# Performance work log

Measured on AMD Instinct MI355X. Metric: run time of the kernel, lower is better.

## Reference

```python
import jax, jax.numpy as jnp
import numpy as np


def setup_inputs() -> dict:
    key = jax.random.key(0)
    ks = jax.random.split(key, 7)
    b, t, c = 2, 2048, 1024
    s = 0.02  # keep pre-softmax logits in a sane range
    return {
        "query": jax.random.normal(ks[0], (b, t, c), jnp.float32),
        "key": jax.random.normal(ks[1], (b, t, c), jnp.float32),
        "value": jax.random.normal(ks[2], (b, t, c), jnp.float32),
        "in_proj_w": jax.random.normal(ks[3], (3 * c, c), jnp.float32) * s,
        "in_proj_b": jax.random.normal(ks[4], (3 * c,), jnp.float32) * s,
        "out_proj_w": jax.random.normal(ks[5], (c, c), jnp.float32) * s,
        "out_proj_b": jax.random.normal(ks[6], (c,), jnp.float32) * s,
        "window_size": 128,
    }


def reference(query, key, value, in_proj_w, in_proj_b, out_proj_w, out_proj_b, window_size):
    num_heads = 16
    b, t, c = query.shape
    hd = c // num_heads
    wq, wk, wv = in_proj_w[:c], in_proj_w[c:2 * c], in_proj_w[2 * c:]
    bq, bk, bv = in_proj_b[:c], in_proj_b[c:2 * c], in_proj_b[2 * c:]
    # project and split heads: [b, h, t, hd]
    q = (query @ wq.T + bq).reshape(b, t, num_heads, hd).transpose(0, 2, 1, 3)
    k = (key @ wk.T + bk).reshape(b, t, num_heads, hd).transpose(0, 2, 1, 3)
    v = (value @ wv.T + bv).reshape(b, t, num_heads, hd).transpose(0, 2, 1, 3)
    # NOTE: torch adds a *float* attn_mask to the logits. The original mask is
    # 1.0 inside the sliding window, 0.0 outside -- an additive +1 bias, NOT -inf.
    idx = jnp.arange(t)
    band = (jnp.abs(idx[:, None] - idx[None, :]) <= window_size).astype(q.dtype)  # [t, t]
    scale = 1.0 / jnp.sqrt(jnp.asarray(hd, q.dtype))
    logits = jnp.einsum("bhqd,bhkd->bhqk", q * scale, k) + band  # [b,h,t,t]
    attn = jax.nn.softmax(logits, axis=-1)
    out = jnp.einsum("bhqk,bhkd->bhqd", attn, v)  # [b,h,t,hd]
    out = out.transpose(0, 2, 1, 3).reshape(b, t, c)
    return out @ out_proj_w.T + out_proj_b
```

## Files before the change

### kernel.cpp

```cpp
#include <hip/hip_runtime.h>

typedef __attribute__((ext_vector_type(8)))  short short8;
typedef __attribute__((ext_vector_type(4)))  float f32x4;
typedef __attribute__((ext_vector_type(16))) float f32x16;

constexpr int B  = 2;
constexpr int T  = 2048;
constexpr int C  = 1024;
constexpr int H  = 16;
constexpr int HD = 64;

__device__ inline unsigned bf16rne(float a){
  unsigned u = __builtin_bit_cast(unsigned, a);
  u += 0x7fffu + ((u >> 16) & 1u);
  return u >> 16;
}
__device__ inline unsigned bf16pair(float a, float b){
  unsigned ua = __builtin_bit_cast(unsigned, a); ua += 0x7fffu + ((ua >> 16) & 1u);
  unsigned ub = __builtin_bit_cast(unsigned, b); ub += 0x7fffu + ((ub >> 16) & 1u);
  return (ua >> 16) | (ub & 0xffff0000u);
}
__device__ inline void gll16(const void* g, void* l){
  __builtin_amdgcn_global_load_lds(
      (const __attribute__((address_space(1))) unsigned*)g,
      (__attribute__((address_space(3))) unsigned*)l, 16, 0, 0);
}
__device__ inline float exp2f_(float x){
#if __has_builtin(__builtin_amdgcn_exp2f)
  return __builtin_amdgcn_exp2f(x);
#else
  return __builtin_exp2f(x);
#endif
}

__global__ void convert_k(const float* __restrict__ ipw, const float* __restrict__ opw,
                          const float* __restrict__ q, const float* __restrict__ k,
                          const float* __restrict__ v, unsigned* __restrict__ dst)
{
  const int i = blockIdx.x * 256 + threadIdx.x;
  const long e = (long)i * 4;
  const float* src; long off;
  if      (e <  3145728) { src = ipw; off = e; }
  else if (e <  4194304) { src = opw; off = e - 3145728; }
  else if (e <  8388608) { src = q;   off = e - 4194304; }
  else if (e < 12582912) { src = k;   off = e - 8388608; }
  else                   { src = v;   off = e - 12582912; }
  const float4 x = *(const float4*)(src + off);
  dst[i*2+0] = bf16pair(x.x, x.y);
  dst[i*2+1] = bf16pair(x.z, x.w);
}

template<int MODE>
__global__ __launch_bounds__(256, 2) void gemm_k(
    const unsigned short* __restrict__ A0, const unsigned short* __restrict__ A1,
    const unsigned short* __restrict__ A2,
    const unsigned short* __restrict__ Wb, const float* __restrict__ bias,
    unsigned short* __restrict__ Qb, unsigned short* __restrict__ Kf,
    unsigned short* __restrict__ Vf, float* __restrict__ outF)
{
  __shared__ __align__(16) char gsm[32768];
  unsigned short* As = (unsigned short*)gsm;
  unsigned short* Bs = (unsigned short*)(gsm + 16384);

  const int tid  = threadIdx.x, lane = tid & 63, wv = tid >> 6;
  const int wm   = wv & 1, wn = wv >> 1;
  const int bn   = blockIdx.x, bm = blockIdx.y;
  const int m16  = lane & 15, quad = lane >> 4;

  const int which = (MODE == 0) ? (bn >> 3) : 0;
  const unsigned short* A = (which == 0) ? A0 : (which == 1 ? A1 : A2);

  f32x4 acc[4][4];
#pragma unroll
  for (int i = 0; i < 4; i++)
#pragma unroll
    for (int j = 0; j < 4; j++) acc[i][j] = (f32x4){0.f, 0.f, 0.f, 0.f};

  const int srow = (lane >> 3);
  const int skp  = (lane & 7) * 8;

  for (int k0 = 0; k0 < 1024; k0 += 64) {
    __syncthreads();
#pragma unroll
    for (int p = 0; p < 4; p++) {
      const int row = wv*32 + p*8 + srow;
      gll16(A  + (size_t)(bm*128 + row)*1024 + k0 + skp, (char*)As + (wv*4+p)*1024);
      gll16(Wb + (size_t)(bn*128 + row)*1024 + k0 + skp, (char*)Bs + (wv*4+p)*1024);
    }
    __syncthreads();

    short8 af[2][4], bf2[2][4];
#pragma unroll
    for (int kh = 0; kh < 2; kh++) {
#pragma unroll
      for (int i = 0; i < 4; i++)
        af[kh][i] = *(const short8*)((const char*)As + (wm*64 + i*16 + m16)*128 + kh*64 + quad*16);
#pragma unroll
      for (int j = 0; j < 4; j++)
        bf2[kh][j] = *(const short8*)((const char*)Bs + (wn*64 + j*16 + m16)*128 + kh*64 + quad*16);
    }
#pragma unroll
    for (int kh = 0; kh < 2; kh++)
#pragma unroll
      for (int i = 0; i < 4; i++)
#pragma unroll
        for (int j = 0; j < 4; j++)
          acc[i][j] = __builtin_amdgcn_mfma_f32_16x16x32_bf16(af[kh][i], bf2[kh][j], acc[i][j], 0,0,0);
  }

  if constexpr (MODE == 1) {
#pragma unroll
    for (int j = 0; j < 4; j++) {
      const int n_e = bn*128 + wn*64 + j*16 + m16;
      const float bj = bias[n_e];
#pragma unroll
      for (int i = 0; i < 4; i++) {
        const int mbase = bm*128 + wm*64 + i*16 + quad*4;
#pragma unroll
        for (int r = 0; r < 4; r++)
          outF[(size_t)(mbase + r) * 1024 + n_e] = acc[i][j][r] + bj;
      }
    }
  } else {
    __syncthreads();
    float* Ls = (float*)gsm;
    const int hbase = (bn & 7) * 2;
    const int b = bm >> 4;
    const int tbase = (bm & 15) * 128;
    if (which < 2) {
#pragma unroll
      for (int j = 0; j < 4; ++j) {
        const float bj = bias[bn*128 + wn*64 + j*16 + m16];
#pragma unroll
        for (int i = 0; i < 4; ++i) {
          const int m0 = wm*64 + i*16 + quad*4;
#pragma unroll
          for (int r = 0; r < 4; ++r)
            Ls[(m0 + r)*36 + wn*16 + m16] = acc[i][j][r] + bj;
        }
        __syncthreads();
#pragma unroll
        for (int r2 = 0; r2 < 2; ++r2) {
          const int v = r2*256 + tid;
          const int m = v & 127, seg = v >> 7;
          const int wn2 = seg >> 1;
          const float* src = &Ls[m*36 + wn2*16 + (seg & 1)*8];
          const float4 f0 = *(const float4*)src;
          const float4 f1 = *(const float4*)(src + 4);
          uint4 st;
          st.x = bf16pair(f0.x, f0.y); st.y = bf16pair(f0.z, f0.w);
          st.z = bf16pair(f1.x, f1.y); st.w = bf16pair(f1.z, f1.w);
          const int bhh = b*16 + hbase + wn2;
          if (which == 0) {
            const int d0 = j*16 + (seg & 1)*8;
            *(uint4*)&Qb[((size_t)(bhh*2048) + tbase + m)*64 + d0] = st;
          } else {
            const int kt = (tbase + m) >> 6;
            const int wkk = (m >> 5) & 1, ln2 = m & 31;
            const int h2 = seg & 1;
            uint4* dp = (uint4*)Kf + ((size_t)(bhh*32 + kt)*8 + j*2 + wkk)*64 + h2*32 + ln2;
            *dp = st;
          }
        }
        __syncthreads();
      }
    } else {
#pragma unroll
      for (int j = 0; j < 4; ++j) {
        const float bj = bias[bn*128 + wn*64 + j*16 + m16];
        const int col = wn*16 + m16;
#pragma unroll
        for (int i = 0; i < 4; ++i) {
          f32x4 tv = acc[i][j];
          tv[0] += bj; tv[1] += bj; tv[2] += bj; tv[3] += bj;
          *(f32x4*)&Ls[col*132 + wm*64 + i*16 + quad*4] = tv;
        }
        __syncthreads();
#pragma unroll
        for (int r2 = 0; r2 < 2; ++r2) {
          const int v = r2*256 + tid;
          const int n = v >> 4, mseg = v & 15;
          const float* src = &Ls[n*132 + mseg*8];
          const float4 f0 = *(const float4*)src;
          const float4 f1 = *(const float4*)(src + 4);
          uint4 st;
          st.x = bf16pair(f0.x, f0.y); st.y = bf16pair(f0.z, f0.w);
          st.z = bf16pair(f1.x, f1.y); st.w = bf16pair(f1.z, f1.w);
          const int d = j*16 + (n & 15);
          const int bhh = b*16 + hbase + (n >> 4);
          const int t0 = tbase + mseg*8;
          const int kt = t0 >> 6, tc = (t0 & 63) >> 3;
          const int wkk = tc >> 2, cc = (tc >> 1) & 1, h2 = tc & 1;
          const int dt = d >> 5, ln2 = d & 31;
          uint4* dp = (uint4*)Vf + (size_t)(bhh*32 + kt)*512 + dt*256 + cc*128 + wkk*64 + h2*32 + ln2;
          *dp = st;
        }
        __syncthreads();
      }
    }
  }
}

__global__ __launch_bounds__(256, 2) void attn_k(
    const unsigned short* __restrict__ Qb, const unsigned short* __restrict__ Kf,
    const unsigned short* __restrict__ Vf, const int* __restrict__ wptr,
    unsigned short* __restrict__ ctx)
{
  __shared__ __align__(16) char smem[16896];
  float* Om   = (float*)smem;
  float* lbuf = (float*)(smem + 16384);

  const int tid = threadIdx.x, lane = tid & 63, wv = tid >> 6;
  const int wq = wv >> 1, wk = wv & 1;
  const int h = lane >> 5, ln = lane & 31;
  const bool hs = (h == 1);
  const int bh = blockIdx.x, qt = blockIdx.y;
  const int win = *wptr;
  const int q0 = qt * 64 + wq * 32;
  const size_t hb = (size_t)bh * T * HD;

  constexpr float LOG2E = 1.44269504f;
  constexpr float C1    = 0.125f * LOG2E;

  short8 qf[4];
#pragma unroll
  for (int s = 0; s < 4; s++)
    qf[s] = *(const short8*)(Qb + hb + (size_t)(q0 + ln)*64 + s*16 + h*8);

  short8 onesv;
#pragma unroll
  for (int jj = 0; jj < 8; jj++) onesv[jj] = (short)0x3F80;

  f32x16 O0, O1, Lacc, Zv;
#pragma unroll
  for (int r = 0; r < 16; r++) { O0[r] = 0.f; O1[r] = 0.f; Lacc[r] = 0.f; Zv[r] = 0.f; }
  const int tq = q0 + ln;

  const uint4* kbase = (const uint4*)Kf + (size_t)bh*32*512 + wk*64 + lane;
  const uint4* vbase = (const uint4*)Vf + (size_t)bh*32*512 + wk*64 + lane;

  uint4 kA[4], vA[4], kB[4], vB[4];
#pragma unroll
  for (int s = 0; s < 4; s++) kA[s] = kbase[s*128];
#pragma unroll
  for (int u = 0; u < 4; u++) vA[u] = vbase[(u >> 1)*256 + (u & 1)*128];

  auto body = [&](int kt, uint4 (&ka)[4], uint4 (&va)[4]) {
    f32x16 st;
#pragma unroll
    for (int s = 0; s < 4; s++) {
      const short8 kf2 = __builtin_bit_cast(short8, ka[s]);
      st = __builtin_amdgcn_mfma_f32_32x32x16_bf16(kf2, qf[s], (s == 0 ? Zv : st), 0, 0, 0);
    }

    const int kb = kt*64 + wk*32;
    int sep = 0;
    if (kb > q0 + 31) sep = kb - (q0 + 31);
    else if (q0 > kb + 31) sep = q0 - (kb + 31);
    const int d1 = kb + 31 - q0, d2 = q0 + 31 - kb;
    const int dmax = max(d1 < 0 ? -d1 : d1, d2 < 0 ? -d2 : d2);

    float pr[16];
    if (sep > win) {
#pragma unroll
      for (int r = 0; r < 16; r++) pr[r] = exp2f_(st[r] * C1);
    } else if (dmax <= win) {
#pragma unroll
      for (int r = 0; r < 16; r++) pr[r] = exp2f_(__builtin_fmaf(st[r], C1, LOG2E));
    } else {
      const int tkb = kb + 4*h;
#pragma unroll
      for (int r = 0; r < 16; r++) {
        const int tk = tkb + (r & 3) + 8*(r >> 2);
        int dd = tq - tk; dd = dd < 0 ? -dd : dd;
        pr[r] = exp2f_(__builtin_fmaf(st[r], C1, dd <= win ? LOG2E : 0.0f));
      }
    }

    unsigned pk[8];
#pragma unroll
    for (int g = 0; g < 8; g++)
      pk[g] = __builtin_amdgcn_perm(__builtin_bit_cast(unsigned, pr[2*g+1]),
                                    __builtin_bit_cast(unsigned, pr[2*g]),
                                    0x07060302u);

#pragma unroll
    for (int c = 0; c < 2; c++) {
      const unsigned sh0 = (unsigned)__shfl_xor((int)pk[4*c+0], 32, 64);
      const unsigned sh1 = (unsigned)__shfl_xor((int)pk[4*c+1], 32, 64);
      const unsigned sh2 = (unsigned)__shfl_xor((int)pk[4*c+2], 32, 64);
      const unsigned sh3 = (unsigned)__shfl_xor((int)pk[4*c+3], 32, 64);
      union { unsigned u[4]; short8 v; } P;
      P.u[0] = hs ? sh2 : pk[4*c+0];
      P.u[1] = hs ? sh3 : pk[4*c+1];
      P.u[2] = hs ? pk[4*c+2] : sh0;
      P.u[3] = hs ? pk[4*c+3] : sh1;
#pragma unroll
      for (int dt = 0; dt < 2; dt++) {
        const short8 vf2 = __builtin_bit_cast(short8, va[dt*2 + c]);
        if (dt == 0) O0 = __builtin_amdgcn_mfma_f32_32x32x16_bf16(P.v, vf2, O0, 0,0,0);
        else         O1 = __builtin_amdgcn_mfma_f32_32x32x16_bf16(P.v, vf2, O1, 0,0,0);
      }
      Lacc = __builtin_amdgcn_mfma_f32_32x32x16_bf16(P.v, onesv, Lacc, 0,0,0);
    }
  };

  for (int kt = 0; kt < 32; kt += 2) {
    {
      const size_t o = (size_t)(kt + 1) * 512;
#pragma unroll
      for (int s = 0; s < 4; s++) kB[s] = kbase[o + s*128];
#pragma unroll
      for (int u = 0; u < 4; u++) vB[u] = vbase[o + (u >> 1)*256 + (u & 1)*128];
    }
    body(kt, kA, vA);
    if (kt + 2 < 32) {
      const size_t o = (size_t)(kt + 2) * 512;
#pragma unroll
      for (int s = 0; s < 4; s++) kA[s] = kbase[o + s*128];
#pragma unroll
      for (int u = 0; u < 4; u++) vA[u] = vbase[o + (u >> 1)*256 + (u & 1)*128];
    }
    body(kt + 1, kB, vB);
  }

  __syncthreads();
  if (wk == 1) {
#pragma unroll
    for (int r = 0; r < 16; r++) {
      Om[wq*2048 + r*64 + lane]        = O0[r];
      Om[wq*2048 + (16 + r)*64 + lane] = O1[r];
    }
    if (ln == 0) {
#pragma unroll
      for (int r = 0; r < 16; r++)
        lbuf[wq*32 + (r & 3) + 8*(r >> 2) + 4*h] = Lacc[r];
    }
  }
  __syncthreads();
  if (wk == 0) {
    const int b = bh >> 4, hh = bh & 15;
#pragma unroll
    for (int r = 0; r < 16; r++) {
      const int qrow = (r & 3) + 8*(r >> 2) + 4*h;
      const float lt = Lacc[r] + lbuf[wq*32 + qrow];
      const float linv = 1.0f / lt;
      const int t = q0 + qrow;
      const float o0 = (O0[r] + Om[wq*2048 + r*64 + lane]) * linv;
      const float o1 = (O1[r] + Om[wq*2048 + (16 + r)*64 + lane]) * linv;
      unsigned short* cp = ctx + (size_t)(b*2048 + t)*1024 + hh*64;
      cp[ln]      = (unsigned short)bf16rne(o0);
      cp[32 + ln] = (unsigned short)bf16rne(o1);
    }
  }
}

extern "C" void kernel_launch(void* const* d_in, const int* in_sizes, int n_in,
                              void* d_out, int out_size, void* d_ws, size_t ws_size,
                              hipStream_t stream)
{
  const float* query = (const float*)d_in[0];
  const float* key   = (const float*)d_in[1];
  const float* value = (const float*)d_in[2];
  const float* ipw   = (const float*)d_in[3];
  const float* ipb   = (const float*)d_in[4];
  const float* opw   = (const float*)d_in[5];
  const float* opb   = (const float*)d_in[6];
  const int*   win   = (const int*)d_in[7];

  char* ws = (char*)d_ws;
  unsigned short* Winbf  = (unsigned short*)(ws);
  unsigned short* Woutbf = (unsigned short*)(ws + 6291456);
  unsigned short* Qin    = (unsigned short*)(ws + 8388608);
  unsigned short* Kin    = (unsigned short*)(ws + 16777216);
  unsigned short* Vin    = (unsigned short*)(ws + 25165824);
  unsigned short* Qb     = (unsigned short*)(ws + 33554432);
  unsigned short* Kf     = (unsigned short*)(ws + 41943040);
  unsigned short* Vf     = (unsigned short*)(ws + 50331648);
  unsigned short* ctx    = (unsigned short*)(ws + 58720256);

  convert_k<<<16384, 256, 0, stream>>>(ipw, opw, query, key, value, (unsigned*)ws);

  gemm_k<0><<<dim3(24, 32), 256, 0, stream>>>(
      Qin, Kin, Vin, Winbf, ipb, Qb, Kf, Vf, nullptr);

  attn_k<<<dim3(32, 32), 256, 0, stream>>>(Qb, Kf, Vf, win, ctx);

  gemm_k<1><<<dim3(8, 32), 256, 0, stream>>>(
      ctx, ctx, ctx, Woutbf, opb, nullptr, nullptr, nullptr, (float*)d_out);
}
```

Baseline: 229.8 us.

## Shrink GEMM k-tiles, split out-proj GEMM, fold softmax scale into K, raise occupancy

The QKV GEMM's K step drops from 64 to 32, which cuts LDS to about 19KB, and launch bounds rise to three blocks per CU. The output projection moves to its own kernel with 128x64 tiles, doubling the grid from 256 to 512 blocks so more CUs are busy. The softmax scale times log2e is folded into K and its bias at projection time, which removes a multiply per logit in attention. Attention drops the double-buffered K/V registers in favour of single buffers prefetched within each iteration, freeing registers for higher occupancy at the cost of less latency hiding.

```diff
diff --git a/kernel.cpp b/kernel.cpp
--- a/kernel.cpp
+++ b/kernel.cpp
@@ -50,24 +50,23 @@
   dst[i*2+1] = bf16pair(x.z, x.w);
 }
 
-template<int MODE>
-__global__ __launch_bounds__(256, 2) void gemm_k(
+__global__ __launch_bounds__(256, 3) void gemm_qkv(
     const unsigned short* __restrict__ A0, const unsigned short* __restrict__ A1,
     const unsigned short* __restrict__ A2,
     const unsigned short* __restrict__ Wb, const float* __restrict__ bias,
     unsigned short* __restrict__ Qb, unsigned short* __restrict__ Kf,
-    unsigned short* __restrict__ Vf, float* __restrict__ outF)
+    unsigned short* __restrict__ Vf)
 {
-  __shared__ __align__(16) char gsm[32768];
+  __shared__ __align__(16) char gsm[18944];
   unsigned short* As = (unsigned short*)gsm;
-  unsigned short* Bs = (unsigned short*)(gsm + 16384);
+  unsigned short* Bs = (unsigned short*)(gsm + 8192);
 
   const int tid  = threadIdx.x, lane = tid & 63, wv = tid >> 6;
   const int wm   = wv & 1, wn = wv >> 1;
   const int bn   = blockIdx.x, bm = blockIdx.y;
   const int m16  = lane & 15, quad = lane >> 4;
 
-  const int which = (MODE == 0) ? (bn >> 3) : 0;
+  const int which = bn >> 3;
   const unsigned short* A = (which == 0) ? A0 : (which == 1 ? A1 : A2);
 
   f32x4 acc[4][4];
@@ -76,132 +75,172 @@
 #pragma unroll
     for (int j = 0; j < 4; j++) acc[i][j] = (f32x4){0.f, 0.f, 0.f, 0.f};
 
-  const int srow = (lane >> 3);
-  const int skp  = (lane & 7) * 8;
-
-  for (int k0 = 0; k0 < 1024; k0 += 64) {
+  const int srow = wv * 32 + (lane >> 2);
+  const int skp  = (lane & 3) * 8;
+
+  for (int k0 = 0; k0 < 1024; k0 += 32) {
     __syncthreads();
 #pragma unroll
-    for (int p = 0; p < 4; p++) {
-      const int row = wv*32 + p*8 + srow;
-      gll16(A  + (size_t)(bm*128 + row)*1024 + k0 + skp, (char*)As + (wv*4+p)*1024);
-      gll16(Wb + (size_t)(bn*128 + row)*1024 + k0 + skp, (char*)Bs + (wv*4+p)*1024);
+    for (int p = 0; p < 2; p++) {
+      gll16(A  + (size_t)(bm*128 + srow + p*16)*1024 + k0 + skp, (char*)As + wv*2048 + p*1024);
+      gll16(Wb + (size_t)(bn*128 + srow + p*16)*1024 + k0 + skp, (char*)Bs + wv*2048 + p*1024);
     }
     __syncthreads();
 
-    short8 af[2][4], bf2[2][4];
-#pragma unroll
-    for (int kh = 0; kh < 2; kh++) {
-#pragma unroll
-      for (int i = 0; i < 4; i++)
-        af[kh][i] = *(const short8*)((const char*)As + (wm*64 + i*16 + m16)*128 + kh*64 + quad*16);
+    short8 af[4], bf[4];
+#pragma unroll
+    for (int i = 0; i < 4; i++)
+      af[i] = *(const short8*)((const char*)As + (wm*64 + i*16 + m16)*64 + quad*16);
+#pragma unroll
+    for (int j = 0; j < 4; j++)
+      bf[j] = *(const short8*)((const char*)Bs + (wn*64 + j*16 + m16)*64 + quad*16);
+#pragma unroll
+    for (int i = 0; i < 4; i++)
 #pragma unroll
       for (int j = 0; j < 4; j++)
-        bf2[kh][j] = *(const short8*)((const char*)Bs + (wn*64 + j*16 + m16)*128 + kh*64 + quad*16);
-    }
-#pragma unroll
-    for (int kh = 0; kh < 2; kh++)
-#pragma unroll
-      for (int i = 0; i < 4; i++)
-#pragma unroll
-        for (int j = 0; j < 4; j++)
-          acc[i][j] = __builtin_amdgcn_mfma_f32_16x16x32_bf16(af[kh][i], bf2[kh][j], acc[i][j], 0,0,0);
-  }
-
-  if constexpr (MODE == 1) {
-#pragma unroll
-    for (int j = 0; j < 4; j++) {
-      const int n_e = bn*128 + wn*64 + j*16 + m16;
-      const float bj = bias[n_e];
-#pragma unroll
-      for (int i = 0; i < 4; i++) {
-        const int mbase = bm*128 + wm*64 + i*16 + quad*4;
-#pragma unroll
-        for (int r = 0; r < 4; r++)
-          outF[(size_t)(mbase + r) * 1024 + n_e] = acc[i][j][r] + bj;
-      }
-    }
-  } else {
-    __syncthreads();
-    float* Ls = (float*)gsm;
-    const int hbase = (bn & 7) * 2;
-    const int b = bm >> 4;
-    const int tbase = (bm & 15) * 128;
-    if (which < 2) {
-#pragma unroll
-      for (int j = 0; j < 4; ++j) {
-        const float bj = bias[bn*128 + wn*64 + j*16 + m16];
-#pragma unroll
-        for (int i = 0; i < 4; ++i) {
-          const int m0 = wm*64 + i*16 + quad*4;
-#pragma unroll
-          for (int r = 0; r < 4; ++r)
-            Ls[(m0 + r)*36 + wn*16 + m16] = acc[i][j][r] + bj;
-        }
-        __syncthreads();
-#pragma unroll
-        for (int r2 = 0; r2 < 2; ++r2) {
-          const int v = r2*256 + tid;
-          const int m = v & 127, seg = v >> 7;
-          const int wn2 = seg >> 1;
-          const float* src = &Ls[m*36 + wn2*16 + (seg & 1)*8];
-          const float4 f0 = *(const float4*)src;
-          const float4 f1 = *(const float4*)(src + 4);
-          uint4 st;
-          st.x = bf16pair(f0.x, f0.y); st.y = bf16pair(f0.z, f0.w);
-          st.z = bf16pair(f1.x, f1.y); st.w = bf16pair(f1.z, f1.w);
-          const int bhh = b*16 + hbase + wn2;
-          if (which == 0) {
-            const int d0 = j*16 + (seg & 1)*8;
-            *(uint4*)&Qb[((size_t)(bhh*2048) + tbase + m)*64 + d0] = st;
-          } else {
-            const int kt = (tbase + m) >> 6;
-            const int wkk = (m >> 5) & 1, ln2 = m & 31;
-            const int h2 = seg & 1;
-            uint4* dp = (uint4*)Kf + ((size_t)(bhh*32 + kt)*8 + j*2 + wkk)*64 + h2*32 + ln2;
-            *dp = st;
-          }
-        }
-        __syncthreads();
-      }
-    } else {
-#pragma unroll
-      for (int j = 0; j < 4; ++j) {
-        const float bj = bias[bn*128 + wn*64 + j*16 + m16];
-        const int col = wn*16 + m16;
-#pragma unroll
-        for (int i = 0; i < 4; ++i) {
-          f32x4 tv = acc[i][j];
-          tv[0] += bj; tv[1] += bj; tv[2] += bj; tv[3] += bj;
-          *(f32x4*)&Ls[col*132 + wm*64 + i*16 + quad*4] = tv;
-        }
-        __syncthreads();
-#pragma unroll
-        for (int r2 = 0; r2 < 2; ++r2) {
-          const int v = r2*256 + tid;
-          const int n = v >> 4, mseg = v & 15;
-          const float* src = &Ls[n*132 + mseg*8];
-          const float4 f0 = *(const float4*)src;
-          const float4 f1 = *(const float4*)(src + 4);
-          uint4 st;
-          st.x = bf16pair(f0.x, f0.y); st.y = bf16pair(f0.z, f0.w);
-          st.z = bf16pair(f1.x, f1.y); st.w = bf16pair(f1.z, f1.w);
-          const int d = j*16 + (n & 15);
-          const int bhh = b*16 + hbase + (n >> 4);
-          const int t0 = tbase + mseg*8;
-          const int kt = t0 >> 6, tc = (t0 & 63) >> 3;
-          const int wkk = tc >> 2, cc = (tc >> 1) & 1, h2 = tc & 1;
-          const int dt = d >> 5, ln2 = d & 31;
-          uint4* dp = (uint4*)Vf + (size_t)(bhh*32 + kt)*512 + dt*256 + cc*128 + wkk*64 + h2*32 + ln2;
+        acc[i][j] = __builtin_amdgcn_mfma_f32_16x16x32_bf16(af[i], bf[j], acc[i][j], 0,0,0);
+  }
+
+  __syncthreads();
+  float* Ls = (float*)gsm;
+  const int hbase = (bn & 7) * 2;
+  const int b = bm >> 4;
+  const int tbase = (bm & 15) * 128;
+  const float ksc = (which == 1) ? 0.18033688f : 1.0f;
+
+  if (which < 2) {
+#pragma unroll
+    for (int j = 0; j < 4; ++j) {
+      const float bj = bias[bn*128 + wn*64 + j*16 + m16] * ksc;
+#pragma unroll
+      for (int i = 0; i < 4; ++i) {
+        const int m0 = wm*64 + i*16 + quad*4;
+#pragma unroll
+        for (int r = 0; r < 4; ++r)
+          Ls[(m0 + r)*36 + wn*16 + m16] = __builtin_fmaf(acc[i][j][r], ksc, bj);
+      }
+      __syncthreads();
+#pragma unroll
+      for (int r2 = 0; r2 < 2; ++r2) {
+        const int v = r2*256 + tid;
+        const int m = v & 127, seg = v >> 7;
+        const int wn2 = seg >> 1;
+        const float* src = &Ls[m*36 + wn2*16 + (seg & 1)*8];
+        const float4 f0 = *(const float4*)src;
+        const float4 f1 = *(const float4*)(src + 4);
+        uint4 st;
+        st.x = bf16pair(f0.x, f0.y); st.y = bf16pair(f0.z, f0.w);
+        st.z = bf16pair(f1.x, f1.y); st.w = bf16pair(f1.z, f1.w);
+        const int bhh = b*16 + hbase + wn2;
+        if (which == 0) {
+          const int d0 = j*16 + (seg & 1)*8;
+          *(uint4*)&Qb[((size_t)(bhh*2048) + tbase + m)*64 + d0] = st;
+        } else {
+          const int kt = (tbase + m) >> 6;
+          const int wkk = (m >> 5) & 1, ln2 = m & 31;
+          const int h2 = seg & 1;
+          uint4* dp = (uint4*)Kf + ((size_t)(bhh*32 + kt)*8 + j*2 + wkk)*64 + h2*32 + ln2;
           *dp = st;
         }
-        __syncthreads();
-      }
-    }
-  }
-}
-
-__global__ __launch_bounds__(256, 2) void attn_k(
+      }
+      __syncthreads();
+    }
+  } else {
+#pragma unroll
+    for (int j = 0; j < 4; ++j) {
+      const float bj = bias[bn*128 + wn*64 + j*16 + m16];
+      const int col = wn*16 + m16;
+#pragma unroll
+      for (int i = 0; i < 4; ++i) {
+        f32x4 tv = acc[i][j];
+        tv[0] += bj; tv[1] += bj; tv[2] += bj; tv[3] += bj;
+        *(f32x4*)&Ls[col*132 + wm*64 + i*16 + quad*4] = tv;
+      }
+      __syncthreads();
+#pragma unroll
+      for (int r2 = 0; r2 < 2; ++r2) {
+        const int v = r2*256 + tid;
+        const int n = v >> 4, mseg = v & 15;
+        const float* src = &Ls[n*132 + mseg*8];
+        const float4 f0 = *(const float4*)src;
+        const float4 f1 = *(const float4*)(src + 4);
+        uint4 st;
+        st.x = bf16pair(f0.x, f0.y); st.y = bf16pair(f0.z, f0.w);
+        st.z = bf16pair(f1.x, f1.y); st.w = bf16pair(f1.z, f1.w);
+        const int d = j*16 + (n & 15);
+        const int bhh = b*16 + hbase + (n >> 4);
+        const int t0 = tbase + mseg*8;
+        const int kt = t0 >> 6, tc = (t0 & 63) >> 3;
+        const int wkk = tc >> 2, cc = (tc >> 1) & 1, h2 = tc & 1;
+        const int dt = d >> 5, ln2 = d & 31;
+        uint4* dp = (uint4*)Vf + (size_t)(bhh*32 + kt)*512 + dt*256 + cc*128 + wkk*64 + h2*32 + ln2;
+        *dp = st;
+      }
+      __syncthreads();
+    }
+  }
+}
+
+__global__ __launch_bounds__(256, 3) void gemm_out(
+    const unsigned short* __restrict__ Ab, const unsigned short* __restrict__ Wb,
+    const float* __restrict__ bias, float* __restrict__ outF)
+{
+  __shared__ __align__(16) char gsm[12288];
+  unsigned short* As = (unsigned short*)gsm;
+  unsigned short* Ws = (unsigned short*)(gsm + 8192);
+
+  const int tid  = threadIdx.x, lane = tid & 63, wv = tid >> 6;
+  const int wm   = wv & 1, wn = wv >> 1;
+  const int bn   = blockIdx.x, bm = blockIdx.y;
+  const int m16  = lane & 15, quad = lane >> 4;
+
+  f32x4 acc[4][2];
+#pragma unroll
+  for (int i = 0; i < 4; i++)
+#pragma unroll
+    for (int j = 0; j < 2; j++) acc[i][j] = (f32x4){0.f, 0.f, 0.f, 0.f};
+
+  const int arow = wv * 32 + (lane >> 2);
+  const int wrow = wv * 16 + (lane >> 2);
+  const int skp  = (lane & 3) * 8;
+
+  for (int k0 = 0; k0 < 1024; k0 += 32) {
+    __syncthreads();
+#pragma unroll
+    for (int p = 0; p < 2; p++)
+      gll16(Ab + (size_t)(bm*128 + arow + p*16)*1024 + k0 + skp, (char*)As + wv*2048 + p*1024);
+    gll16(Wb + (size_t)(bn*64 + wrow)*1024 + k0 + skp, (char*)Ws + wv*1024);
+    __syncthreads();
+
+    short8 af[4], bf[2];
+#pragma unroll
+    for (int i = 0; i < 4; i++)
+      af[i] = *(const short8*)((const char*)As + (wm*64 + i*16 + m16)*64 + quad*16);
+#pragma unroll
+    for (int j = 0; j < 2; j++)
+      bf[j] = *(const short8*)((const char*)Ws + (wn*32 + j*16 + m16)*64 + quad*16);
+#pragma unroll
+    for (int i = 0; i < 4; i++)
+#pragma unroll
+      for (int j = 0; j < 2; j++)
+        acc[i][j] = __builtin_amdgcn_mfma_f32_16x16x32_bf16(af[i], bf[j], acc[i][j], 0,0,0);
+  }
+
+#pragma unroll
+  for (int j = 0; j < 2; j++) {
+    const int n_e = bn*64 + wn*32 + j*16 + m16;
+    const float bj = bias[n_e];
+#pragma unroll
+    for (int i = 0; i < 4; i++) {
+      const int mbase = bm*128 + wm*64 + i*16 + quad*4;
+#pragma unroll
+      for (int r = 0; r < 4; r++)
+        outF[(size_t)(mbase + r) * 1024 + n_e] = acc[i][j][r] + bj;
+    }
+  }
+}
+
+__global__ __launch_bounds__(256, 3) void attn_k(
     const unsigned short* __restrict__ Qb, const unsigned short* __restrict__ Kf,
     const unsigned short* __restrict__ Vf, const int* __restrict__ wptr,
     unsigned short* __restrict__ ctx)
@@ -220,7 +259,6 @@
   const size_t hb = (size_t)bh * T * HD;
 
   constexpr float LOG2E = 1.44269504f;
-  constexpr float C1    = 0.125f * LOG2E;
 
   short8 qf[4];
 #pragma unroll
@@ -239,18 +277,23 @@
   const uint4* kbase = (const uint4*)Kf + (size_t)bh*32*512 + wk*64 + lane;
   const uint4* vbase = (const uint4*)Vf + (size_t)bh*32*512 + wk*64 + lane;
 
-  uint4 kA[4], vA[4], kB[4], vB[4];
+  uint4 kA[4], vA[4];
 #pragma unroll
   for (int s = 0; s < 4; s++) kA[s] = kbase[s*128];
 #pragma unroll
   for (int u = 0; u < 4; u++) vA[u] = vbase[(u >> 1)*256 + (u & 1)*128];
 
-  auto body = [&](int kt, uint4 (&ka)[4], uint4 (&va)[4]) {
+  for (int kt = 0; kt < 32; ++kt) {
     f32x16 st;
 #pragma unroll
     for (int s = 0; s < 4; s++) {
-      const short8 kf2 = __builtin_bit_cast(short8, ka[s]);
+      const short8 kf2 = __builtin_bit_cast(short8, kA[s]);
       st = __builtin_amdgcn_mfma_f32_32x32x16_bf16(kf2, qf[s], (s == 0 ? Zv : st), 0, 0, 0);
+    }
+    if (kt < 31) {
+      const size_t o = (size_t)(kt + 1) * 512;
+#pragma unroll
+      for (int s = 0; s < 4; s++) kA[s] = kbase[o + s*128];
     }
 
     const int kb = kt*64 + wk*32;
@@ -263,17 +306,17 @@
     float pr[16];
     if (sep > win) {
 #pragma unroll
-      for (int r = 0; r < 16; r++) pr[r] = exp2f_(st[r] * C1);
+      for (int r = 0; r < 16; r++) pr[r] = exp2f_(st[r]);
     } else if (dmax <= win) {
 #pragma unroll
-      for (int r = 0; r < 16; r++) pr[r] = exp2f_(__builtin_fmaf(st[r], C1, LOG2E));
+      for (int r = 0; r < 16; r++) pr[r] = exp2f_(st[r] + LOG2E);
     } else {
       const int tkb = kb + 4*h;
 #pragma unroll
       for (int r = 0; r < 16; r++) {
         const int tk = tkb + (r & 3) + 8*(r >> 2);
         int dd = tq - tk; dd = dd < 0 ? -dd : dd;
-        pr[r] = exp2f_(__builtin_fmaf(st[r], C1, dd <= win ? LOG2E : 0.0f));
+        pr[r] = exp2f_(st[r] + (dd <= win ? LOG2E : 0.0f));
       }
     }
 
@@ -297,31 +340,18 @@
       P.u[3] = hs ? pk[4*c+3] : sh1;
 #pragma unroll
       for (int dt = 0; dt < 2; dt++) {
-        const short8 vf2 = __builtin_bit_cast(short8, va[dt*2 + c]);
+        const short8 vf2 = __builtin_bit_cast(short8, vA[dt*2 + c]);
         if (dt == 0) O0 = __builtin_amdgcn_mfma_f32_32x32x16_bf16(P.v, vf2, O0, 0,0,0);
         else         O1 = __builtin_amdgcn_mfma_f32_32x32x16_bf16(P.v, vf2, O1, 0,0,0);
       }
       Lacc = __builtin_amdgcn_mfma_f32_32x32x16_bf16(P.v, onesv, Lacc, 0,0,0);
     }
-  };
-
-  for (int kt = 0; kt < 32; kt += 2) {
-    {
+
+    if (kt < 31) {
       const size_t o = (size_t)(kt + 1) * 512;
 #pragma unroll
-      for (int s = 0; s < 4; s++) kB[s] = kbase[o + s*128];
-#pragma unroll
-      for (int u = 0; u < 4; u++) vB[u] = vbase[o + (u >> 1)*256 + (u & 1)*128];
-    }
-    body(kt, kA, vA);
-    if (kt + 2 < 32) {
-      const size_t o = (size_t)(kt + 2) * 512;
-#pragma unroll
-      for (int s = 0; s < 4; s++) kA[s] = kbase[o + s*128];
-#pragma unroll
       for (int u = 0; u < 4; u++) vA[u] = vbase[o + (u >> 1)*256 + (u & 1)*128];
     }
-    body(kt + 1, kB, vB);
   }
 
   __syncthreads();
@@ -381,11 +411,11 @@
 
   convert_k<<<16384, 256, 0, stream>>>(ipw, opw, query, key, value, (unsigned*)ws);
 
-  gemm_k<0><<<dim3(24, 32), 256, 0, stream>>>(
-      Qin, Kin, Vin, Winbf, ipb, Qb, Kf, Vf, nullptr);
+  gemm_qkv<<<dim3(24, 32), 256, 0, stream>>>(
+      Qin, Kin, Vin, Winbf, ipb, Qb, Kf, Vf);
 
   attn_k<<<dim3(32, 32), 256, 0, stream>>>(Qb, Kf, Vf, win, ctx);
 
-  gemm_k<1><<<dim3(8, 32), 256, 0, stream>>>(
-      ctx, ctx, ctx, Woutbf, opb, nullptr, nullptr, nullptr, (float*)d_out);
-}
+  gemm_out<<<dim3(16, 32), 256, 0, stream>>>(
+      ctx, Woutbf, opb, (float*)d_out);
+}
```

Result: no change. 226.2 us (-1.6%).
